# Kernel optimization log

Measured on AMD Instinct MI355X. Metric: run time of the kernel, lower is better.

Reference implementation:

```python
import jax, jax.numpy as jnp
import numpy as np

B, T, C, H = 4, 2048, 1024, 16
D = C // H  # head_dim = 64


def setup_inputs() -> dict:
    key = jax.random.key(0)
    k1, k2, k3, k4, k5 = jax.random.split(key, 5)
    x = jax.random.normal(k1, (B, T, C), dtype=jnp.float32)
    # torch nn.Linear weights: [out_features, in_features]
    s = 1.0 / np.sqrt(C)
    qkv_w = jax.random.uniform(k2, (3 * C, C), dtype=jnp.float32, minval=-s, maxval=s)
    qkv_b = jax.random.uniform(k3, (3 * C,), dtype=jnp.float32, minval=-s, maxval=s)
    out_w = jax.random.uniform(k4, (C, C), dtype=jnp.float32, minval=-s, maxval=s)
    out_b = jax.random.uniform(k5, (C,), dtype=jnp.float32, minval=-s, maxval=s)
    # causal mask broadcastable to [B,H,T,T]; 0 (False) marks masked positions
    attn_mask = jnp.tril(jnp.ones((T, T), dtype=bool))[None, None]
    return {"x": x, "qkv_w": qkv_w, "qkv_b": qkv_b, "out_w": out_w,
            "out_b": out_b, "attn_mask": attn_mask}


def reference(x, qkv_w, qkv_b, out_w, out_b, attn_mask):
    qkv = x @ qkv_w.T + qkv_b                      # [B,T,3C]
    q, k, v = jnp.split(qkv, 3, axis=-1)
    # [B,T,C] -> [B,H,T,D]
    q = q.reshape(B, T, H, D).transpose(0, 2, 1, 3)
    k = k.reshape(B, T, H, D).transpose(0, 2, 1, 3)
    v = v.reshape(B, T, H, D).transpose(0, 2, 1, 3)
    scale = 1.0 / np.sqrt(D)
    attn = jnp.einsum('bhqd,bhkd->bhqk', q, k) * scale   # [B,H,T,T]
    neg = jnp.finfo(attn.dtype).min
    attn = jnp.where(attn_mask, attn, neg)
    attn = jax.nn.softmax(attn, axis=-1)
    out = jnp.einsum('bhqk,bhkd->bhqd', attn, v)          # [B,H,T,D]
    out = out.transpose(0, 2, 1, 3).reshape(B, T, C)
    return out @ out_w.T + out_b
```

## Files before the change

### kernel.cpp

```cpp
#include <hip/hip_runtime.h>
#include <hip/hip_bf16.h>

#define B_ 4
#define T_ 2048
#define C_ 1024
#define H_ 16
#define D_ 64

typedef __hip_bfloat16 bf16;
typedef float f32x4 __attribute__((ext_vector_type(4)));
typedef short bf16s8 __attribute__((ext_vector_type(8)));

#define NEG_BIG (-1e30f)

__device__ inline unsigned short f2bf(float f) {
  __hip_bfloat16 h = __float2bfloat16(f);
  return *reinterpret_cast<unsigned short*>(&h);
}
__device__ inline float bf_lo(unsigned u) {
  union { unsigned u; float f; } c; c.u = u << 16; return c.f;
}

__device__ inline void async_load16(const void* g, void* l) {
  __builtin_amdgcn_global_load_lds(
      (const __attribute__((address_space(1))) unsigned int*)g,
      (__attribute__((address_space(3))) unsigned int*)l, 16, 0, 0);
}

__device__ inline void plswap32(unsigned& a, unsigned& b) {
  auto r = __builtin_amdgcn_permlane32_swap(a, b, false, false);
  a = r[0]; b = r[1];
}
__device__ inline void plswap16(unsigned& a, unsigned& b) {
  auto r = __builtin_amdgcn_permlane16_swap(a, b, false, false);
  a = r[0]; b = r[1];
}

__device__ inline void pk_to_frags(const unsigned pk[4][2], bf16s8& p0, bf16s8& p1) {
  union { unsigned w[4]; bf16s8 v; } u0, u1;
  unsigned a, b2;
  a = pk[0][0]; b2 = pk[1][0]; plswap32(a, b2); plswap16(a, b2); u0.w[0] = a; u0.w[2] = b2;
  a = pk[0][1]; b2 = pk[1][1]; plswap32(a, b2); plswap16(a, b2); u0.w[1] = a; u0.w[3] = b2;
  a = pk[2][0]; b2 = pk[3][0]; plswap32(a, b2); plswap16(a, b2); u1.w[0] = a; u1.w[2] = b2;
  a = pk[2][1]; b2 = pk[3][1]; plswap32(a, b2); plswap16(a, b2); u1.w[1] = a; u1.w[3] = b2;
  p0 = u0.v; p1 = u1.v;
}

union U4 { uint4 u; unsigned short s[8]; };

__device__ inline uint4 load8(const void* base, size_t idx, int f32) {
  if (f32) {
    const float* p = (const float*)base + idx;
    float4 a = *(const float4*)p;
    float4 b = *(const float4*)(p + 4);
    U4 r;
    r.s[0] = f2bf(a.x); r.s[1] = f2bf(a.y); r.s[2] = f2bf(a.z); r.s[3] = f2bf(a.w);
    r.s[4] = f2bf(b.x); r.s[5] = f2bf(b.y); r.s[6] = f2bf(b.z); r.s[7] = f2bf(b.w);
    return r.u;
  }
  return *(const uint4*)((const unsigned short*)base + idx);
}

__global__ void detect_k(const unsigned short* __restrict__ w, int* __restrict__ flag) {
  int lane = threadIdx.x;
  bool big = false;
  for (int i = lane; i < 512; i += 64) {
    float f = bf_lo((unsigned)w[i]);
    if (!(fabsf(f) <= 1.0f)) big = true;
  }
  int any = __any(big);
  if (lane == 0) *flag = any ? 1 : 0;
}

#define R_X   1048576
#define R_WQ  (R_X + 393216)
#define R_WO  (R_WQ + 131072)
#define R_BQ  (R_WO + 384)
#define R_BO  (R_BQ + 128)
__global__ __launch_bounds__(256) void convert_all_k(
    const void* __restrict__ x, const void* __restrict__ wq,
    const void* __restrict__ wo, const void* __restrict__ bq,
    const void* __restrict__ bo,
    bf16* __restrict__ xd, bf16* __restrict__ wqd, bf16* __restrict__ wod,
    bf16* __restrict__ bqd, bf16* __restrict__ bod,
    const int* __restrict__ flag) {
  const int f32 = *flag;
  long long g = (long long)blockIdx.x * 256 + threadIdx.x;
  if (g >= R_BO) return;
  const void* src; bf16* dst; long long base;
  if (g < R_X)       { src = x;  dst = xd;  base = 0; }
  else if (g < R_WQ) { src = wq; dst = wqd; base = R_X; }
  else if (g < R_WO) { src = wo; dst = wod; base = R_WQ; }
  else if (g < R_BQ) { src = bq; dst = bqd; base = R_WO; }
  else               { src = bo; dst = bod; base = R_BQ; }
  size_t i = (size_t)(g - base) * 8;
  *(uint4*)(dst + i) = load8(src, i, f32);
}

template <int KDIM, int MROWS>
__device__ inline void gemm_core(const bf16* __restrict__ A,
                                 const bf16* __restrict__ W,
                                 int tm, int tn, int wm, int wn,
                                 f32x4 acc[MROWS / 32][4], bf16* As, bf16* Bs) {
  const int tid  = threadIdx.x;
  const int lane = tid & 63;
  const int rl   = lane & 15;
  const int kq   = (lane >> 4) * 8;

  for (int k0 = 0; k0 < KDIM; k0 += 32) {
    __syncthreads();
#pragma unroll
    for (int j = 0; j < MROWS / 64; ++j) {
      int f    = j * 4096 + tid * 16;
      int row  = f >> 6;
      int colb = f & 63;
      async_load16((const char*)A + ((size_t)(tm + row) * KDIM + k0) * 2 + colb,
                   (char*)As + f);
    }
#pragma unroll
    for (int j = 0; j < 2; ++j) {
      int f    = j * 4096 + tid * 16;
      int row  = f >> 6;
      int colb = f & 63;
      async_load16((const char*)W + ((size_t)(tn + row) * KDIM + k0) * 2 + colb,
                   (char*)Bs + f);
    }
    __syncthreads();

    bf16s8 af[MROWS / 32], bw[4];
#pragma unroll
    for (int mt = 0; mt < MROWS / 32; ++mt)
      af[mt] = *(const bf16s8*)(As + (wm + mt * 16 + rl) * 32 + kq);
#pragma unroll
    for (int nt = 0; nt < 4; ++nt)
      bw[nt] = *(const bf16s8*)(Bs + (wn + nt * 16 + rl) * 32 + kq);

#pragma unroll
    for (int mt = 0; mt < MROWS / 32; ++mt)
#pragma unroll
      for (int nt = 0; nt < 4; ++nt)
        acc[mt][nt] = __builtin_amdgcn_mfma_f32_16x16x32_bf16(af[mt], bw[nt],
                                                              acc[mt][nt], 0, 0, 0);
  }
}

#define CSTRIDE 72
#define FSTRIDE 68

__global__ __launch_bounds__(256) void gemm_qkv_k(
    const bf16* __restrict__ X, const bf16* __restrict__ W,
    const bf16* __restrict__ bias,
    bf16* __restrict__ q, bf16* __restrict__ k, bf16* __restrict__ v) {
  __shared__ __align__(16) char smem[4 * 64 * CSTRIDE * 2];
  bf16* As = (bf16*)smem;
  bf16* Bs = (bf16*)(smem + 8192);
  const int tid = threadIdx.x;
  const int wave = tid >> 6, lane = tid & 63;
  const int tm = blockIdx.x * 128, tn = blockIdx.y * 128;
  const int wm = (wave >> 1) * 64, wn = (wave & 1) * 64;
  f32x4 acc[4][4];
#pragma unroll
  for (int i = 0; i < 4; ++i)
#pragma unroll
    for (int j = 0; j < 4; ++j) acc[i][j] = 0.0f;

  gemm_core<C_, 128>(X, W, tm, tn, wm, wn, acc, As, Bs);

  __syncthreads();
  bf16* Cs = (bf16*)smem + wave * 64 * CSTRIDE;

  const int rl = lane & 15, qd = lane >> 4;
  const int nbase = tn + wn;
  const int which = nbase >> 10;
  const int h = (nbase & 1023) >> 6;
  const float sc = which == 0 ? 0.125f : 1.0f;
  const int mbase = tm + wm;
  const int b = mbase >> 11, t0 = mbase & 2047;
  bf16* dst = which == 0 ? q : (which == 1 ? k : v);
  bf16* base = dst + (((size_t)(b * H_ + h)) * T_ + t0) * D_;

#pragma unroll
  for (int nt = 0; nt < 4; ++nt) {
    float bv = __bfloat162float(bias[nbase + nt * 16 + rl]);
#pragma unroll
    for (int mt = 0; mt < 4; ++mt)
#pragma unroll
      for (int r = 0; r < 4; ++r)
        Cs[(mt * 16 + qd * 4 + r) * CSTRIDE + nt * 16 + rl] =
            __float2bfloat16((acc[mt][nt][r] + bv) * sc);
  }
#pragma unroll
  for (int it = 0; it < 8; ++it) {
    int row = it * 8 + (lane >> 3);
    uint4 val = *(const uint4*)(Cs + row * CSTRIDE + (lane & 7) * 8);
    *(uint4*)(base + row * D_ + (lane & 7) * 8) = val;
  }
}

__global__ __launch_bounds__(256) void gemm_out_k(
    const bf16* __restrict__ O, const bf16* __restrict__ W,
    const bf16* __restrict__ bias, const int* __restrict__ flag,
    void* __restrict__ out) {
  __shared__ __align__(16) char smem[4 * 32 * FSTRIDE * 4];
  bf16* As = (bf16*)smem;
  bf16* Bs = (bf16*)(smem + 4096);
  const int f32 = *flag;
  const int tid = threadIdx.x;
  const int wave = tid >> 6, lane = tid & 63;
  const int tm = blockIdx.x * 64, tn = blockIdx.y * 128;
  const int wm = (wave >> 1) * 32, wn = (wave & 1) * 64;
  f32x4 acc[2][4];
#pragma unroll
  for (int i = 0; i < 2; ++i)
#pragma unroll
    for (int j = 0; j < 4; ++j) acc[i][j] = 0.0f;

  gemm_core<C_, 64>(O, W, tm, tn, wm, wn, acc, As, Bs);

  __syncthreads();
  const int rl = lane & 15, qd = lane >> 4;

  if (f32) {
    float* Cs = (float*)(smem + wave * 32 * FSTRIDE * 4);
#pragma unroll
    for (int nt = 0; nt < 4; ++nt) {
      float bv = __bfloat162float(bias[tn + wn + nt * 16 + rl]);
#pragma unroll
      for (int mt = 0; mt < 2; ++mt)
#pragma unroll
        for (int r = 0; r < 4; ++r)
          Cs[(mt * 16 + qd * 4 + r) * FSTRIDE + nt * 16 + rl] = acc[mt][nt][r] + bv;
    }
    float* obase = (float*)out + (size_t)(tm + wm) * C_ + tn + wn;
#pragma unroll
    for (int it = 0; it < 8; ++it) {
      int row = it * 4 + (lane >> 4);
      float4 val = *(const float4*)(Cs + row * FSTRIDE + (lane & 15) * 4);
      *(float4*)(obase + (size_t)row * C_ + (lane & 15) * 4) = val;
    }
  } else {
    bf16* Cs = (bf16*)(smem + wave * 32 * FSTRIDE * 4);
#pragma unroll
    for (int nt = 0; nt < 4; ++nt) {
      float bv = __bfloat162float(bias[tn + wn + nt * 16 + rl]);
#pragma unroll
      for (int mt = 0; mt < 2; ++mt)
#pragma unroll
        for (int r = 0; r < 4; ++r)
          Cs[(mt * 16 + qd * 4 + r) * CSTRIDE + nt * 16 + rl] =
              __float2bfloat16(acc[mt][nt][r] + bv);
    }
    bf16* obase = (bf16*)out + (size_t)(tm + wm) * C_ + tn + wn;
#pragma unroll
    for (int it = 0; it < 4; ++it) {
      int row = it * 8 + (lane >> 3);
      uint4 val = *(const uint4*)(Cs + row * CSTRIDE + (lane & 7) * 8);
      *(uint4*)(obase + (size_t)row * C_ + (lane & 7) * 8) = val;
    }
  }
}

__global__ __launch_bounds__(256) void fattn_k(
    const bf16* __restrict__ q, const bf16* __restrict__ k,
    const bf16* __restrict__ v, bf16* __restrict__ o) {
  __shared__ __align__(16) bf16 Ks[2][64 * 64];
  __shared__ __align__(16) bf16 Vs[2][64 * 64];
  const int tid = threadIdx.x, wave = tid >> 6, lane = tid & 63;
  const int rl = lane & 15, quad = lane >> 4;
  const int bh = blockIdx.x;
  const int b = bh >> 4, h = bh & 15;
  const size_t bhT = (size_t)bh * T_;
  const int sw0 = (quad ^ (rl & 7)) << 3;
  const int sw1 = ((quad | 4) ^ (rl & 7)) << 3;

  bf16s8 ones;
#pragma unroll
  for (int i = 0; i < 8; ++i) ones[i] = (short)0x3F80;

  const int y = blockIdx.y;
  const int qbb = (y & 12) | (((y & 3) + (y >> 2)) & 3);
  const int q0 = qbb * 128;

  const int kr0 = tid >> 3;
  const int kc0 = ((tid & 7) ^ (kr0 & 7)) << 4;
  const char* kstage = (const char*)k + (bhT + kr0) * (D_ * 2) + kc0;

  const int kp = tid & 31, dg = tid >> 5;
  const bf16* vstage = v + (bhT + 2 * kp) * D_ + dg * 8;

  const int t0a = q0 + wave * 32;
  const int t0b = t0a + 16;
  const bf16* qra = q + (bhT + t0a + rl) * D_;
  bf16s8 qf0a = *(const bf16s8*)(qra + quad * 8);
  bf16s8 qf1a = *(const bf16s8*)(qra + 32 + quad * 8);
  bf16s8 qf0b = *(const bf16s8*)(qra + 16 * D_ + quad * 8);
  bf16s8 qf1b = *(const bf16s8*)(qra + 16 * D_ + 32 + quad * 8);

  f32x4 oaccA[4], oaccB[4], laccA, laccB;
#pragma unroll
  for (int nt = 0; nt < 4; ++nt) { oaccA[nt] = 0.0f; oaccB[nt] = 0.0f; }
  laccA = 0.0f; laccB = 0.0f;

  const int nchunk = 2 * qbb + 2;

  {
    async_load16(kstage, (char*)Ks[0] + tid * 16);
    async_load16(kstage + 32 * 128, (char*)Ks[0] + 4096 + tid * 16);
    uint4 va = *(const uint4*)(vstage);
    uint4 vb = *(const uint4*)(vstage + D_);
    const unsigned* au = (const unsigned*)&va;
    const unsigned* bu = (const unsigned*)&vb;
#pragma unroll
    for (int m = 0; m < 4; ++m) {
      unsigned lo = (au[m] & 0xffffu) | (bu[m] << 16);
      unsigned hi = (au[m] >> 16) | (bu[m] & 0xffff0000u);
      int d0 = dg * 8 + 2 * m;
      int o0 = d0 * 64 + (((kp >> 2) ^ (2 * m)) << 3) + 2 * (kp & 3);
      int o1 = (d0 + 1) * 64 + (((kp >> 2) ^ (2 * m + 1)) << 3) + 2 * (kp & 3);
      *(unsigned*)(Vs[0] + o0) = lo;
      *(unsigned*)(Vs[0] + o1) = hi;
    }
  }
  __syncthreads();

  int cur = 0;
#pragma unroll 1
  for (int c = 0; c < nchunk; ++c) {
    const bf16* Kc = Ks[cur];
    const bf16* Vc = Vs[cur];
    const bool pf = (c + 1 < nchunk);

    uint4 va, vb;
    if (pf) {
      const char* ks = kstage + (size_t)(c + 1) * 8192;
      char* kd = (char*)Ks[cur ^ 1] + tid * 16;
      async_load16(ks, kd);
      async_load16(ks + 32 * 128, kd + 4096);
      const bf16* vs = vstage + (size_t)(c + 1) * 4096;
      va = *(const uint4*)(vs);
      vb = *(const uint4*)(vs + D_);
    }

    const int k0 = c << 6;

    if (k0 <= t0a + 15) {
      f32x4 sA[4], sB[4];
#pragma unroll
      for (int nt = 0; nt < 4; ++nt) { sA[nt] = 0.0f; sB[nt] = 0.0f; }
#pragma unroll
      for (int nt = 0; nt < 4; ++nt) {
        int key = nt * 16 + rl;
        bf16s8 kb0 = *(const bf16s8*)(Kc + key * 64 + sw0);
        bf16s8 kb1 = *(const bf16s8*)(Kc + key * 64 + sw1);
        sA[nt] = __builtin_amdgcn_mfma_f32_16x16x32_bf16(kb0, qf0a, sA[nt], 0, 0, 0);
        sA[nt] = __builtin_amdgcn_mfma_f32_16x16x32_bf16(kb1, qf1a, sA[nt], 0, 0, 0);
        sB[nt] = __builtin_amdgcn_mfma_f32_16x16x32_bf16(kb0, qf0b, sB[nt], 0, 0, 0);
        sB[nt] = __builtin_amdgcn_mfma_f32_16x16x32_bf16(kb1, qf1b, sB[nt], 0, 0, 0);
      }

      if (k0 + 63 > t0a) {
        int t = t0a + rl;
#pragma unroll
        for (int nt = 0; nt < 4; ++nt)
#pragma unroll
          for (int r = 0; r < 4; ++r) {
            int key = k0 + nt * 16 + quad * 4 + r;
            if (key > t) sA[nt][r] = NEG_BIG;
          }
      }
      if (k0 + 63 > t0b) {
        int t = t0b + rl;
#pragma unroll
        for (int nt = 0; nt < 4; ++nt)
#pragma unroll
          for (int r = 0; r < 4; ++r) {
            int key = k0 + nt * 16 + quad * 4 + r;
            if (key > t) sB[nt][r] = NEG_BIG;
          }
      }

      unsigned pkA[4][2], pkB[4][2];
#pragma unroll
      for (int nt = 0; nt < 4; ++nt) {
#pragma unroll
        for (int r = 0; r < 4; ++r) {
          sA[nt][r] = __expf(fminf(sA[nt][r], 30.0f));
          sB[nt][r] = __expf(fminf(sB[nt][r], 30.0f));
        }
        pkA[nt][0] = (unsigned)f2bf(sA[nt][0]) | ((unsigned)f2bf(sA[nt][1]) << 16);
        pkA[nt][1] = (unsigned)f2bf(sA[nt][2]) | ((unsigned)f2bf(sA[nt][3]) << 16);
        pkB[nt][0] = (unsigned)f2bf(sB[nt][0]) | ((unsigned)f2bf(sB[nt][1]) << 16);
        pkB[nt][1] = (unsigned)f2bf(sB[nt][2]) | ((unsigned)f2bf(sB[nt][3]) << 16);
      }

      bf16s8 paA0, paA1, paB0, paB1;
      pk_to_frags(pkA, paA0, paA1);
      pk_to_frags(pkB, paB0, paB1);

      laccA = __builtin_amdgcn_mfma_f32_16x16x32_bf16(paA0, ones, laccA, 0, 0, 0);
      laccA = __builtin_amdgcn_mfma_f32_16x16x32_bf16(paA1, ones, laccA, 0, 0, 0);
      laccB = __builtin_amdgcn_mfma_f32_16x16x32_bf16(paB0, ones, laccB, 0, 0, 0);
      laccB = __builtin_amdgcn_mfma_f32_16x16x32_bf16(paB1, ones, laccB, 0, 0, 0);

#pragma unroll
      for (int nt = 0; nt < 4; ++nt) {
        int d = nt * 16 + rl;
        bf16s8 vb0 = *(const bf16s8*)(Vc + d * 64 + sw0);
        bf16s8 vb1 = *(const bf16s8*)(Vc + d * 64 + sw1);
        oaccA[nt] = __builtin_amdgcn_mfma_f32_16x16x32_bf16(paA0, vb0, oaccA[nt], 0, 0, 0);
        oaccA[nt] = __builtin_amdgcn_mfma_f32_16x16x32_bf16(paA1, vb1, oaccA[nt], 0, 0, 0);
        oaccB[nt] = __builtin_amdgcn_mfma_f32_16x16x32_bf16(paB0, vb0, oaccB[nt], 0, 0, 0);
        oaccB[nt] = __builtin_amdgcn_mfma_f32_16x16x32_bf16(paB1, vb1, oaccB[nt], 0, 0, 0);
      }
    }

    if (pf) {
      bf16* Vn = Vs[cur ^ 1];
      const unsigned* au = (const unsigned*)&va;
      const unsigned* bu = (const unsigned*)&vb;
#pragma unroll
      for (int m = 0; m < 4; ++m) {
        unsigned lo = (au[m] & 0xffffu) | (bu[m] << 16);
        unsigned hi = (au[m] >> 16) | (bu[m] & 0xffff0000u);
        int d0 = dg * 8 + 2 * m;
        int o0 = d0 * 64 + (((kp >> 2) ^ (2 * m)) << 3) + 2 * (kp & 3);
        int o1 = (d0 + 1) * 64 + (((kp >> 2) ^ (2 * m + 1)) << 3) + 2 * (kp & 3);
        *(unsigned*)(Vn + o0) = lo;
        *(unsigned*)(Vn + o1) = hi;
      }
    }
    __syncthreads();
    cur ^= 1;
  }

  f32x4 linvA, linvB;
#pragma unroll
  for (int r = 0; r < 4; ++r) {
    linvA[r] = 1.0f / laccA[r];
    linvB[r] = 1.0f / laccB[r];
  }
#pragma unroll
  for (int nt = 0; nt < 4; ++nt) {
    int d = nt * 16 + rl;
#pragma unroll
    for (int r = 0; r < 4; ++r) {
      int tA = t0a + quad * 4 + r;
      int tB = t0b + quad * 4 + r;
      o[((size_t)b * T_ + tA) * C_ + h * D_ + d] =
          __float2bfloat16(oaccA[nt][r] * linvA[r]);
      o[((size_t)b * T_ + tB) * C_ + h * D_ + d] =
          __float2bfloat16(oaccB[nt][r] * linvB[r]);
    }
  }
}

extern "C" void kernel_launch(void* const* d_in, const int* in_sizes, int n_in,
                              void* d_out, int out_size, void* d_ws, size_t ws_size,
                              hipStream_t stream) {
  (void)in_sizes; (void)n_in; (void)out_size; (void)ws_size;
  const void* x     = d_in[0];
  const void* qkv_w = d_in[1];
  const void* qkv_b = d_in[2];
  const void* out_w = d_in[3];
  const void* out_b = d_in[4];

  const size_t nqkv = (size_t)B_ * T_ * C_;
  char* ws = (char*)d_ws;
  int*  flag = (int*)ws;
  bf16* q   = (bf16*)(ws + 256);
  bf16* kk  = q + nqkv;
  bf16* vv  = kk + nqkv;
  bf16* oo  = vv + nqkv;
  bf16* xbf = oo;
  bf16* wqkv = oo + nqkv;
  bf16* wout = wqkv + 3 * C_ * C_;
  bf16* bqkv = wout + C_ * C_;
  bf16* bout = bqkv + 3 * C_;

  detect_k<<<1, 64, 0, stream>>>((const unsigned short*)qkv_w, flag);
  convert_all_k<<<(R_BO + 255) / 256, 256, 0, stream>>>(
      x, qkv_w, out_w, qkv_b, out_b, xbf, wqkv, wout, bqkv, bout, flag);

  gemm_qkv_k<<<dim3(64, 24), 256, 0, stream>>>(xbf, wqkv, bqkv, q, kk, vv);
  fattn_k<<<dim3(64, 16), 256, 0, stream>>>(q, kk, vv, oo);
  gemm_out_k<<<dim3(128, 8), 256, 0, stream>>>(oo, wout, bout, flag, d_out);
}
```

Baseline: 286.5 us.

## Halve attention block to two waves over 64 queries, launch heaviest blocks first

The flash-attention kernel now uses 128-thread blocks, each covering 64 query rows instead of 128, and the grid doubles to 32 query blocks per head. Blocks are ordered in reverse so the longest causal rows are scheduled first, replacing the old swizzled pairing. Each thread now stages twice as much K/V per chunk, and the per-wave skip of fully masked chunks is removed because it can no longer trigger. The intent is finer-grained, better-balanced work across CUs with more resident blocks. The cost is more K/V reloading per query and fewer waves sharing each staged tile.

```diff
diff --git a/kernel.cpp b/kernel.cpp
--- a/kernel.cpp
+++ b/kernel.cpp
@@ -44,6 +44,21 @@
   a = pk[2][0]; b2 = pk[3][0]; plswap32(a, b2); plswap16(a, b2); u1.w[0] = a; u1.w[2] = b2;
   a = pk[2][1]; b2 = pk[3][1]; plswap32(a, b2); plswap16(a, b2); u1.w[1] = a; u1.w[3] = b2;
   p0 = u0.v; p1 = u1.v;
+}
+
+__device__ inline void v_transpose_write(bf16* Vn, uint4 va, uint4 vb, int kp, int dgrp) {
+  const unsigned* au = (const unsigned*)&va;
+  const unsigned* bu = (const unsigned*)&vb;
+#pragma unroll
+  for (int m = 0; m < 4; ++m) {
+    unsigned lo = (au[m] & 0xffffu) | (bu[m] << 16);
+    unsigned hi = (au[m] >> 16) | (bu[m] & 0xffff0000u);
+    int d0 = dgrp * 8 + 2 * m;
+    int o0 = d0 * 64 + (((kp >> 2) ^ (2 * m)) << 3) + 2 * (kp & 3);
+    int o1 = (d0 + 1) * 64 + (((kp >> 2) ^ (2 * m + 1)) << 3) + 2 * (kp & 3);
+    *(unsigned*)(Vn + o0) = lo;
+    *(unsigned*)(Vn + o1) = hi;
+  }
 }
 
 union U4 { uint4 u; unsigned short s[8]; };
@@ -260,7 +275,7 @@
   }
 }
 
-__global__ __launch_bounds__(256) void fattn_k(
+__global__ __launch_bounds__(128) void fattn_k(
     const bf16* __restrict__ q, const bf16* __restrict__ k,
     const bf16* __restrict__ v, bf16* __restrict__ o) {
   __shared__ __align__(16) bf16 Ks[2][64 * 64];
@@ -277,9 +292,8 @@
 #pragma unroll
   for (int i = 0; i < 8; ++i) ones[i] = (short)0x3F80;
 
-  const int y = blockIdx.y;
-  const int qbb = (y & 12) | (((y & 3) + (y >> 2)) & 3);
-  const int q0 = qbb * 128;
+  const int qb = 31 - blockIdx.y;
+  const int q0 = qb * 64;
 
   const int kr0 = tid >> 3;
   const int kc0 = ((tid & 7) ^ (kr0 & 7)) << 4;
@@ -301,25 +315,20 @@
   for (int nt = 0; nt < 4; ++nt) { oaccA[nt] = 0.0f; oaccB[nt] = 0.0f; }
   laccA = 0.0f; laccB = 0.0f;
 
-  const int nchunk = 2 * qbb + 2;
+  const int nchunk = qb + 1;
 
   {
-    async_load16(kstage, (char*)Ks[0] + tid * 16);
-    async_load16(kstage + 32 * 128, (char*)Ks[0] + 4096 + tid * 16);
+    char* kd = (char*)Ks[0] + tid * 16;
+    async_load16(kstage, kd);
+    async_load16(kstage + 2048, kd + 2048);
+    async_load16(kstage + 4096, kd + 4096);
+    async_load16(kstage + 6144, kd + 6144);
     uint4 va = *(const uint4*)(vstage);
     uint4 vb = *(const uint4*)(vstage + D_);
-    const unsigned* au = (const unsigned*)&va;
-    const unsigned* bu = (const unsigned*)&vb;
-#pragma unroll
-    for (int m = 0; m < 4; ++m) {
-      unsigned lo = (au[m] & 0xffffu) | (bu[m] << 16);
-      unsigned hi = (au[m] >> 16) | (bu[m] & 0xffff0000u);
-      int d0 = dg * 8 + 2 * m;
-      int o0 = d0 * 64 + (((kp >> 2) ^ (2 * m)) << 3) + 2 * (kp & 3);
-      int o1 = (d0 + 1) * 64 + (((kp >> 2) ^ (2 * m + 1)) << 3) + 2 * (kp & 3);
-      *(unsigned*)(Vs[0] + o0) = lo;
-      *(unsigned*)(Vs[0] + o1) = hi;
-    }
+    uint4 vc = *(const uint4*)(vstage + 32);
+    uint4 vd = *(const uint4*)(vstage + D_ + 32);
+    v_transpose_write(Vs[0], va, vb, kp, dg);
+    v_transpose_write(Vs[0], vc, vd, kp, dg + 4);
   }
   __syncthreads();
 
@@ -330,104 +339,96 @@
     const bf16* Vc = Vs[cur];
     const bool pf = (c + 1 < nchunk);
 
-    uint4 va, vb;
+    uint4 va, vb, vc, vd;
     if (pf) {
       const char* ks = kstage + (size_t)(c + 1) * 8192;
       char* kd = (char*)Ks[cur ^ 1] + tid * 16;
       async_load16(ks, kd);
-      async_load16(ks + 32 * 128, kd + 4096);
+      async_load16(ks + 2048, kd + 2048);
+      async_load16(ks + 4096, kd + 4096);
+      async_load16(ks + 6144, kd + 6144);
       const bf16* vs = vstage + (size_t)(c + 1) * 4096;
       va = *(const uint4*)(vs);
       vb = *(const uint4*)(vs + D_);
+      vc = *(const uint4*)(vs + 32);
+      vd = *(const uint4*)(vs + D_ + 32);
     }
 
     const int k0 = c << 6;
 
-    if (k0 <= t0a + 15) {
-      f32x4 sA[4], sB[4];
-#pragma unroll
-      for (int nt = 0; nt < 4; ++nt) { sA[nt] = 0.0f; sB[nt] = 0.0f; }
-#pragma unroll
-      for (int nt = 0; nt < 4; ++nt) {
-        int key = nt * 16 + rl;
-        bf16s8 kb0 = *(const bf16s8*)(Kc + key * 64 + sw0);
-        bf16s8 kb1 = *(const bf16s8*)(Kc + key * 64 + sw1);
-        sA[nt] = __builtin_amdgcn_mfma_f32_16x16x32_bf16(kb0, qf0a, sA[nt], 0, 0, 0);
-        sA[nt] = __builtin_amdgcn_mfma_f32_16x16x32_bf16(kb1, qf1a, sA[nt], 0, 0, 0);
-        sB[nt] = __builtin_amdgcn_mfma_f32_16x16x32_bf16(kb0, qf0b, sB[nt], 0, 0, 0);
-        sB[nt] = __builtin_amdgcn_mfma_f32_16x16x32_bf16(kb1, qf1b, sB[nt], 0, 0, 0);
+    f32x4 sA[4], sB[4];
+#pragma unroll
+    for (int nt = 0; nt < 4; ++nt) { sA[nt] = 0.0f; sB[nt] = 0.0f; }
+#pragma unroll
+    for (int nt = 0; nt < 4; ++nt) {
+      int key = nt * 16 + rl;
+      bf16s8 kb0 = *(const bf16s8*)(Kc + key * 64 + sw0);
+      bf16s8 kb1 = *(const bf16s8*)(Kc + key * 64 + sw1);
+      sA[nt] = __builtin_amdgcn_mfma_f32_16x16x32_bf16(kb0, qf0a, sA[nt], 0, 0, 0);
+      sA[nt] = __builtin_amdgcn_mfma_f32_16x16x32_bf16(kb1, qf1a, sA[nt], 0, 0, 0);
+      sB[nt] = __builtin_amdgcn_mfma_f32_16x16x32_bf16(kb0, qf0b, sB[nt], 0, 0, 0);
+      sB[nt] = __builtin_amdgcn_mfma_f32_16x16x32_bf16(kb1, qf1b, sB[nt], 0, 0, 0);
+    }
+
+    if (k0 + 63 > t0a) {
+      int t = t0a + rl;
+#pragma unroll
+      for (int nt = 0; nt < 4; ++nt)
+#pragma unroll
+        for (int r = 0; r < 4; ++r) {
+          int key = k0 + nt * 16 + quad * 4 + r;
+          if (key > t) sA[nt][r] = NEG_BIG;
+        }
+    }
+    if (k0 + 63 > t0b) {
+      int t = t0b + rl;
+#pragma unroll
+      for (int nt = 0; nt < 4; ++nt)
+#pragma unroll
+        for (int r = 0; r < 4; ++r) {
+          int key = k0 + nt * 16 + quad * 4 + r;
+          if (key > t) sB[nt][r] = NEG_BIG;
+        }
+    }
+
+    unsigned pkA[4][2], pkB[4][2];
+#pragma unroll
+    for (int nt = 0; nt < 4; ++nt) {
+#pragma unroll
+      for (int r = 0; r < 4; ++r) {
+        sA[nt][r] = __expf(fminf(sA[nt][r], 30.0f));
+        sB[nt][r] = __expf(fminf(sB[nt][r], 30.0f));
       }
-
-      if (k0 + 63 > t0a) {
-        int t = t0a + rl;
-#pragma unroll
-        for (int nt = 0; nt < 4; ++nt)
-#pragma unroll
-          for (int r = 0; r < 4; ++r) {
-            int key = k0 + nt * 16 + quad * 4 + r;
-            if (key > t) sA[nt][r] = NEG_BIG;
-          }
-      }
-      if (k0 + 63 > t0b) {
-        int t = t0b + rl;
-#pragma unroll
-        for (int nt = 0; nt < 4; ++nt)
-#pragma unroll
-          for (int r = 0; r < 4; ++r) {
-            int key = k0 + nt * 16 + quad * 4 + r;
-            if (key > t) sB[nt][r] = NEG_BIG;
-          }
-      }
-
-      unsigned pkA[4][2], pkB[4][2];
-#pragma unroll
-      for (int nt = 0; nt < 4; ++nt) {
-#pragma unroll
-        for (int r = 0; r < 4; ++r) {
-          sA[nt][r] = __expf(fminf(sA[nt][r], 30.0f));
-          sB[nt][r] = __expf(fminf(sB[nt][r], 30.0f));
-        }
-        pkA[nt][0] = (unsigned)f2bf(sA[nt][0]) | ((unsigned)f2bf(sA[nt][1]) << 16);
-        pkA[nt][1] = (unsigned)f2bf(sA[nt][2]) | ((unsigned)f2bf(sA[nt][3]) << 16);
-        pkB[nt][0] = (unsigned)f2bf(sB[nt][0]) | ((unsigned)f2bf(sB[nt][1]) << 16);
-        pkB[nt][1] = (unsigned)f2bf(sB[nt][2]) | ((unsigned)f2bf(sB[nt][3]) << 16);
-      }
-
-      bf16s8 paA0, paA1, paB0, paB1;
-      pk_to_frags(pkA, paA0, paA1);
-      pk_to_frags(pkB, paB0, paB1);
-
-      laccA = __builtin_amdgcn_mfma_f32_16x16x32_bf16(paA0, ones, laccA, 0, 0, 0);
-      laccA = __builtin_amdgcn_mfma_f32_16x16x32_bf16(paA1, ones, laccA, 0, 0, 0);
-      laccB = __builtin_amdgcn_mfma_f32_16x16x32_bf16(paB0, ones, laccB, 0, 0, 0);
-      laccB = __builtin_amdgcn_mfma_f32_16x16x32_bf16(paB1, ones, laccB, 0, 0, 0);
-
-#pragma unroll
-      for (int nt = 0; nt < 4; ++nt) {
-        int d = nt * 16 + rl;
-        bf16s8 vb0 = *(const bf16s8*)(Vc + d * 64 + sw0);
-        bf16s8 vb1 = *(const bf16s8*)(Vc + d * 64 + sw1);
-        oaccA[nt] = __builtin_amdgcn_mfma_f32_16x16x32_bf16(paA0, vb0, oaccA[nt], 0, 0, 0);
-        oaccA[nt] = __builtin_amdgcn_mfma_f32_16x16x32_bf16(paA1, vb1, oaccA[nt], 0, 0, 0);
-        oaccB[nt] = __builtin_amdgcn_mfma_f32_16x16x32_bf16(paB0, vb0, oaccB[nt], 0, 0, 0);
-        oaccB[nt] = __builtin_amdgcn_mfma_f32_16x16x32_bf16(paB1, vb1, oaccB[nt], 0, 0, 0);
-      }
+      pkA[nt][0] = (unsigned)f2bf(sA[nt][0]) | ((unsigned)f2bf(sA[nt][1]) << 16);
+      pkA[nt][1] = (unsigned)f2bf(sA[nt][2]) | ((unsigned)f2bf(sA[nt][3]) << 16);
+      pkB[nt][0] = (unsigned)f2bf(sB[nt][0]) | ((unsigned)f2bf(sB[nt][1]) << 16);
+      pkB[nt][1] = (unsigned)f2bf(sB[nt][2]) | ((unsigned)f2bf(sB[nt][3]) << 16);
+    }
+
+    bf16s8 paA0, paA1, paB0, paB1;
+    pk_to_frags(pkA, paA0, paA1);
+    pk_to_frags(pkB, paB0, paB1);
+
+    laccA = __builtin_amdgcn_mfma_f32_16x16x32_bf16(paA0, ones, laccA, 0, 0, 0);
+    laccA = __builtin_amdgcn_mfma_f32_16x16x32_bf16(paA1, ones, laccA, 0, 0, 0);
+    laccB = __builtin_amdgcn_mfma_f32_16x16x32_bf16(paB0, ones, laccB, 0, 0, 0);
+    laccB = __builtin_amdgcn_mfma_f32_16x16x32_bf16(paB1, ones, laccB, 0, 0, 0);
+
+#pragma unroll
+    for (int nt = 0; nt < 4; ++nt) {
+      int d = nt * 16 + rl;
+      bf16s8 vb0 = *(const bf16s8*)(Vc + d * 64 + sw0);
+      bf16s8 vb1 = *(const bf16s8*)(Vc + d * 64 + sw1);
+      oaccA[nt] = __builtin_amdgcn_mfma_f32_16x16x32_bf16(paA0, vb0, oaccA[nt], 0, 0, 0);
+      oaccA[nt] = __builtin_amdgcn_mfma_f32_16x16x32_bf16(paA1, vb1, oaccA[nt], 0, 0, 0);
+      oaccB[nt] = __builtin_amdgcn_mfma_f32_16x16x32_bf16(paB0, vb0, oaccB[nt], 0, 0, 0);
+      oaccB[nt] = __builtin_amdgcn_mfma_f32_16x16x32_bf16(paB1, vb1, oaccB[nt], 0, 0, 0);
     }
 
     if (pf) {
       bf16* Vn = Vs[cur ^ 1];
-      const unsigned* au = (const unsigned*)&va;
-      const unsigned* bu = (const unsigned*)&vb;
-#pragma unroll
-      for (int m = 0; m < 4; ++m) {
-        unsigned lo = (au[m] & 0xffffu) | (bu[m] << 16);
-        unsigned hi = (au[m] >> 16) | (bu[m] & 0xffff0000u);
-        int d0 = dg * 8 + 2 * m;
-        int o0 = d0 * 64 + (((kp >> 2) ^ (2 * m)) << 3) + 2 * (kp & 3);
-        int o1 = (d0 + 1) * 64 + (((kp >> 2) ^ (2 * m + 1)) << 3) + 2 * (kp & 3);
-        *(unsigned*)(Vn + o0) = lo;
-        *(unsigned*)(Vn + o1) = hi;
-      }
+      v_transpose_write(Vn, va, vb, kp, dg);
+      v_transpose_write(Vn, vc, vd, kp, dg + 4);
     }
     __syncthreads();
     cur ^= 1;
@@ -482,6 +483,6 @@
       x, qkv_w, out_w, qkv_b, out_b, xbf, wqkv, wout, bqkv, bout, flag);
 
   gemm_qkv_k<<<dim3(64, 24), 256, 0, stream>>>(xbf, wqkv, bqkv, q, kk, vv);
-  fattn_k<<<dim3(64, 16), 256, 0, stream>>>(q, kk, vv, oo);
+  fattn_k<<<dim3(64, 32), 128, 0, stream>>>(q, kk, vv, oo);
   gemm_out_k<<<dim3(128, 8), 256, 0, stream>>>(oo, wout, bout, flag, d_out);
 }
```

Result: no change. 284.1 us (-0.8%).
